# Performance work log

Measured on AMD Instinct MI355X. Metric: run time of the kernel, lower is better.

The kernel has to match this reference:

```python
import jax, jax.numpy as jnp
import numpy as np

N_NODES = 100000
N_EDGES = 1600000
N_IN = 64
N_OUT = 64


def setup_inputs() -> dict:
    key = jax.random.key(0)
    k_x, k_w, k_src, k_dst, k_val = jax.random.split(key, 5)
    X = jax.random.normal(k_x, (N_NODES, N_IN), dtype=jnp.float32)
    # Xavier-uniform init of the GCN weight matrix
    limit = float(np.sqrt(6.0 / (N_IN + N_OUT)))
    W = jax.random.uniform(k_w, (N_IN, N_OUT), dtype=jnp.float32,
                           minval=-limit, maxval=limit)
    # Sparse adjacency A in COO form: out[dst] += val * h[src]
    edge_src = jax.random.randint(k_src, (N_EDGES,), 0, N_NODES, dtype=jnp.int32)
    edge_dst = jax.random.randint(k_dst, (N_EDGES,), 0, N_NODES, dtype=jnp.int32)
    # normalized adjacency values (e.g., 1/sqrt(d_i d_j)); use uniform(0,1)
    edge_val = jax.random.uniform(k_val, (N_EDGES,), dtype=jnp.float32)
    return {"X": X, "W": W, "edge_val": edge_val,
            "edge_src": edge_src, "edge_dst": edge_dst}


def reference(X, W, edge_val, edge_src, edge_dst):
    # dropout p=0.0 -> identity (eval-mode math)
    h = X @ W                                   # [N, n_out] feature transform
    msgs = h[edge_src] * edge_val[:, None]      # [E, n_out] gather + scale
    agg = jax.ops.segment_sum(msgs, edge_dst, num_segments=N_NODES)  # A @ h
    return jax.nn.relu(agg)
```

## Files before the change

kernel.cpp:

```cpp
#include <hip/hip_runtime.h>
#include <hip/hip_bf16.h>

#define N_NODES 100000
#define N_IN    64
#define N_OUT   64
#define N_EDGES 1600000

#define BSHIFT  7
#define NPB     128
#define NB      782
#define CAP     2560
#define P1_EPT  16
#define P1_EPB  (256 * P1_EPT)
#define P1_BLOCKS ((N_EDGES + P1_EPB - 1) / P1_EPB)

__device__ inline unsigned short f2bf(float f) {
    __hip_bfloat16 b = __float2bfloat16(f);
    union { __hip_bfloat16 b; unsigned short u; } c; c.b = b; return c.u;
}

__global__ __launch_bounds__(256) void gemm_bf16_kernel(
        const float* __restrict__ X, const float* __restrict__ W,
        unsigned short* __restrict__ h) {
    __shared__ float Ws[N_IN * N_OUT];
    for (int i = threadIdx.x * 4; i < N_IN * N_OUT; i += 256 * 4)
        *(float4*)&Ws[i] = *(const float4*)&W[i];
    __syncthreads();

    const int r0 = blockIdx.x * 32 + (threadIdx.x >> 4) * 2;
    const int c0 = (threadIdx.x & 15) * 4;

    float acc0[4] = {0.f, 0.f, 0.f, 0.f};
    float acc1[4] = {0.f, 0.f, 0.f, 0.f};
    const float* x0p = X + (size_t)r0 * N_IN;
    const float* x1p = x0p + N_IN;

#pragma unroll 4
    for (int k4 = 0; k4 < 16; ++k4) {
        const float4 x0 = *(const float4*)(x0p + k4 * 4);
        const float4 x1 = *(const float4*)(x1p + k4 * 4);
        const float xa0[4] = {x0.x, x0.y, x0.z, x0.w};
        const float xa1[4] = {x1.x, x1.y, x1.z, x1.w};
#pragma unroll
        for (int kk = 0; kk < 4; ++kk) {
            const float4 w = *(const float4*)&Ws[(k4 * 4 + kk) * N_OUT + c0];
            acc0[0] = fmaf(xa0[kk], w.x, acc0[0]);
            acc0[1] = fmaf(xa0[kk], w.y, acc0[1]);
            acc0[2] = fmaf(xa0[kk], w.z, acc0[2]);
            acc0[3] = fmaf(xa0[kk], w.w, acc0[3]);
            acc1[0] = fmaf(xa1[kk], w.x, acc1[0]);
            acc1[1] = fmaf(xa1[kk], w.y, acc1[1]);
            acc1[2] = fmaf(xa1[kk], w.z, acc1[2]);
            acc1[3] = fmaf(xa1[kk], w.w, acc1[3]);
        }
    }
    ushort4 s0 = {f2bf(acc0[0]), f2bf(acc0[1]), f2bf(acc0[2]), f2bf(acc0[3])};
    ushort4 s1 = {f2bf(acc1[0]), f2bf(acc1[1]), f2bf(acc1[2]), f2bf(acc1[3])};
    *(ushort4*)&h[(size_t)r0 * N_OUT + c0] = s0;
    *(ushort4*)&h[(size_t)(r0 + 1) * N_OUT + c0] = s1;
}

__global__ __launch_bounds__(256) void bucket_kernel(
        const int* __restrict__ edge_src, const int* __restrict__ edge_dst,
        const float* __restrict__ edge_val,
        int* __restrict__ bucket_cursor, int2* __restrict__ staged) {
    __shared__ int cnt[NB];
    __shared__ int base[NB];
    const int t = threadIdx.x;
    for (int i = t; i < NB; i += 256) cnt[i] = 0;
    __syncthreads();

    const int e0 = blockIdx.x * P1_EPB + t * P1_EPT;
    const bool act = (e0 + P1_EPT) <= N_EDGES;
    int bk[P1_EPT], pk[P1_EPT], vv[P1_EPT];

    if (act) {
#pragma unroll
        for (int q = 0; q < P1_EPT / 4; ++q) {
            const int4 d4 = *(const int4*)(edge_dst + e0 + q * 4);
            const int4 s4 = *(const int4*)(edge_src + e0 + q * 4);
            const int4 v4 = *(const int4*)((const int*)edge_val + e0 + q * 4);
            const int da[4] = {d4.x, d4.y, d4.z, d4.w};
            const int sa[4] = {s4.x, s4.y, s4.z, s4.w};
            const int va[4] = {v4.x, v4.y, v4.z, v4.w};
#pragma unroll
            for (int j = 0; j < 4; ++j) {
                const int i = q * 4 + j;
                const int d = da[j];
                bk[i] = d >> BSHIFT;
                pk[i] = sa[j] | ((d & (NPB - 1)) << 17);
                vv[i] = va[j];
                atomicAdd(&cnt[bk[i]], 1);
            }
        }
    }
    __syncthreads();
    for (int i = t; i < NB; i += 256) {
        const int c = cnt[i];
        base[i] = c ? atomicAdd(&bucket_cursor[i], c) : 0;
        cnt[i] = 0;
    }
    __syncthreads();
    if (act) {
#pragma unroll
        for (int i = 0; i < P1_EPT; ++i) {
            const int b = bk[i];
            const int r = atomicAdd(&cnt[b], 1);
            const int pos = base[b] + r;
            if (pos < CAP) {
                int2 o; o.x = pk[i]; o.y = vv[i];
                staged[(size_t)b * CAP + pos] = o;
            }
        }
    }
}

__global__ __launch_bounds__(512) void sort_gather_kernel(
        const unsigned int* __restrict__ h32,
        const int2* __restrict__ staged,
        const int* __restrict__ bucket_cursor,
        float* __restrict__ out) {
    __shared__ int2 srt[CAP];
    __shared__ int  ncnt[NPB];
    __shared__ int  noff[NPB];
    const int t = threadIdx.x;
    const int b = blockIdx.x;
    const int cnt = min(bucket_cursor[b], CAP);
    const int2* bucket = staged + (size_t)b * CAP;

    if (t < NPB) ncnt[t] = 0;
    __syncthreads();
    for (int e = t; e < cnt; e += 512)
        atomicAdd(&ncnt[(unsigned)bucket[e].x >> 17], 1);
    __syncthreads();
    if (t < NPB) noff[t] = ncnt[t];
    __syncthreads();
    for (int d = 1; d < NPB; d <<= 1) {
        int x = 0;
        if (t < NPB && t >= d) x = noff[t - d];
        __syncthreads();
        if (t < NPB) noff[t] += x;
        __syncthreads();
    }
    if (t < NPB) {
        const int excl = noff[t] - ncnt[t];
        noff[t] = excl;
        ncnt[t] = excl;
    }
    __syncthreads();
    for (int e = t; e < cnt; e += 512) {
        const int2 p = bucket[e];
        const int node = (unsigned)p.x >> 17;
        const int pos = atomicAdd(&ncnt[node], 1);
        int2 o; o.x = p.x & 0x1FFFF; o.y = p.y;
        srt[pos] = o;
    }
    __syncthreads();

    const int w   = t >> 6;
    const int hf  = (t >> 5) & 1;
    const int i32 = t & 31;

    for (int nl = w * 16; nl < w * 16 + 16; ++nl) {
        const int node = b * NPB + nl;
        if (node >= N_NODES) break;
        const int s = noff[nl];
        const int e_end = ncnt[nl];

        float a0 = 0.f, a1 = 0.f;
        int e = s + hf;
        for (; e + 2 < e_end; e += 4) {
            const int2 p0 = srt[e];
            const int2 p1 = srt[e + 2];
            const unsigned int w0 = h32[(size_t)p0.x * 32 + i32];
            const unsigned int w1 = h32[(size_t)p1.x * 32 + i32];
            const float v0 = __int_as_float(p0.y);
            const float v1 = __int_as_float(p1.y);
            a0 = fmaf(__uint_as_float(w0 << 16), v0, a0);
            a1 = fmaf(__uint_as_float(w0 & 0xffff0000u), v0, a1);
            a0 = fmaf(__uint_as_float(w1 << 16), v1, a0);
            a1 = fmaf(__uint_as_float(w1 & 0xffff0000u), v1, a1);
        }
        for (; e < e_end; e += 2) {
            const int2 p = srt[e];
            const unsigned int w0 = h32[(size_t)p.x * 32 + i32];
            const float v = __int_as_float(p.y);
            a0 = fmaf(__uint_as_float(w0 << 16), v, a0);
            a1 = fmaf(__uint_as_float(w0 & 0xffff0000u), v, a1);
        }
        a0 += __shfl_xor(a0, 32, 64);
        a1 += __shfl_xor(a1, 32, 64);
        if (hf == 0) {
            float2 o;
            o.x = fmaxf(a0, 0.f);
            o.y = fmaxf(a1, 0.f);
            *(float2*)&out[(size_t)node * 64 + 2 * i32] = o;
        }
    }
}

__global__ __launch_bounds__(256) void gemm_f32_kernel(const float* __restrict__ X,
                                                       const float* __restrict__ W,
                                                       float* __restrict__ h) {
    __shared__ float Ws[N_IN * N_OUT];
    for (int i = threadIdx.x * 4; i < N_IN * N_OUT; i += 256 * 4)
        *(float4*)&Ws[i] = *(const float4*)&W[i];
    __syncthreads();
    const int lane = threadIdx.x & 63;
    const int wid = threadIdx.x >> 6;
    for (int row = blockIdx.x * 4 + wid; row < N_NODES; row += gridDim.x * 4) {
        const float x = X[row * N_IN + lane];
        float acc = 0.0f;
#pragma unroll
        for (int k = 0; k < N_IN; ++k)
            acc = fmaf(__shfl(x, k), Ws[k * N_OUT + lane], acc);
        h[row * N_OUT + lane] = acc;
    }
}

__global__ __launch_bounds__(256) void scatter_kernel(const float* __restrict__ h,
                                                      const float* __restrict__ edge_val,
                                                      const int* __restrict__ edge_src,
                                                      const int* __restrict__ edge_dst,
                                                      float* __restrict__ out) {
    const int lane = threadIdx.x & 63;
    const int e = (int)((blockIdx.x * 256u + threadIdx.x) >> 6);
    if (e >= N_EDGES) return;
    const float m = h[(size_t)edge_src[e] * N_OUT + lane] * edge_val[e];
    atomicAdd(&out[(size_t)edge_dst[e] * N_OUT + lane], m);
}

__global__ __launch_bounds__(256) void relu_kernel(float* __restrict__ out, int n) {
    const int i = (int)(blockIdx.x * 256u + threadIdx.x) * 4;
    if (i + 3 < n) {
        float4 v = *(float4*)&out[i];
        v.x = fmaxf(v.x, 0.f); v.y = fmaxf(v.y, 0.f);
        v.z = fmaxf(v.z, 0.f); v.w = fmaxf(v.w, 0.f);
        *(float4*)&out[i] = v;
    }
}

extern "C" void kernel_launch(void* const* d_in, const int* in_sizes, int n_in,
                              void* d_out, int out_size, void* d_ws, size_t ws_size,
                              hipStream_t stream) {
    const float* X        = (const float*)d_in[0];
    const float* W        = (const float*)d_in[1];
    const float* edge_val = (const float*)d_in[2];
    const int*   edge_src = (const int*)d_in[3];
    const int*   edge_dst = (const int*)d_in[4];
    float*       out      = (float*)d_out;

    unsigned short* h   = (unsigned short*)d_ws;
    int2* staged        = (int2*)((char*)d_ws + (size_t)N_NODES * N_OUT * 2);
    int*  bucket_cursor = (int*)(staged + (size_t)NB * CAP);
    const size_t need = (size_t)((char*)(bucket_cursor + NB) - (char*)d_ws);

    if (ws_size >= need) {
        hipMemsetAsync(bucket_cursor, 0, NB * sizeof(int), stream);
        gemm_bf16_kernel<<<N_NODES / 32, 256, 0, stream>>>(X, W, h);
        bucket_kernel<<<P1_BLOCKS, 256, 0, stream>>>(edge_src, edge_dst, edge_val,
                                                     bucket_cursor, staged);
        sort_gather_kernel<<<NB, 512, 0, stream>>>((const unsigned int*)h, staged,
                                                   bucket_cursor, out);
    } else {
        float* hf = (float*)d_ws;
        hipMemsetAsync(d_out, 0, (size_t)out_size * sizeof(float), stream);
        gemm_f32_kernel<<<25000, 256, 0, stream>>>(X, W, hf);
        const long long st = (long long)N_EDGES * 64;
        scatter_kernel<<<(int)((st + 255) / 256), 256, 0, stream>>>(
            hf, edge_val, edge_src, edge_dst, out);
        relu_kernel<<<(out_size / 4 + 255) / 256, 256, 0, stream>>>(out, out_size);
    }
}
```

Measured before the change: 173.4 us.

## Merge GEMM and bucketing into one launch; unroll gather loop deeper

The bf16 feature-transform GEMM and the edge bucketing pass are combined into a single prep kernel whose blocks branch on block index, with the bucketing blocks reusing the GEMM's shared weight buffer for their counters. This removes one kernel launch and lets the two independent phases run concurrently on the GPU instead of back to back. Separately, the gather loop in the sort/gather kernel is unrolled from two to four edges per iteration per half-wave, so more independent h loads are in flight. The wider unroll raises register pressure, and the mixed block types may balance unevenly across compute units.

```diff
diff --git a/kernel.cpp b/kernel.cpp
--- a/kernel.cpp
+++ b/kernel.cpp
@@ -13,103 +13,106 @@
 #define P1_EPT  16
 #define P1_EPB  (256 * P1_EPT)
 #define P1_BLOCKS ((N_EDGES + P1_EPB - 1) / P1_EPB)
+#define GEMM_BLOCKS (N_NODES / 32)
 
 __device__ inline unsigned short f2bf(float f) {
     __hip_bfloat16 b = __float2bfloat16(f);
     union { __hip_bfloat16 b; unsigned short u; } c; c.b = b; return c.u;
 }
 
-__global__ __launch_bounds__(256) void gemm_bf16_kernel(
+__global__ __launch_bounds__(256) void prep_kernel(
         const float* __restrict__ X, const float* __restrict__ W,
-        unsigned short* __restrict__ h) {
-    __shared__ float Ws[N_IN * N_OUT];
-    for (int i = threadIdx.x * 4; i < N_IN * N_OUT; i += 256 * 4)
-        *(float4*)&Ws[i] = *(const float4*)&W[i];
-    __syncthreads();
-
-    const int r0 = blockIdx.x * 32 + (threadIdx.x >> 4) * 2;
-    const int c0 = (threadIdx.x & 15) * 4;
-
-    float acc0[4] = {0.f, 0.f, 0.f, 0.f};
-    float acc1[4] = {0.f, 0.f, 0.f, 0.f};
-    const float* x0p = X + (size_t)r0 * N_IN;
-    const float* x1p = x0p + N_IN;
-
-#pragma unroll 4
-    for (int k4 = 0; k4 < 16; ++k4) {
-        const float4 x0 = *(const float4*)(x0p + k4 * 4);
-        const float4 x1 = *(const float4*)(x1p + k4 * 4);
-        const float xa0[4] = {x0.x, x0.y, x0.z, x0.w};
-        const float xa1[4] = {x1.x, x1.y, x1.z, x1.w};
-#pragma unroll
-        for (int kk = 0; kk < 4; ++kk) {
-            const float4 w = *(const float4*)&Ws[(k4 * 4 + kk) * N_OUT + c0];
-            acc0[0] = fmaf(xa0[kk], w.x, acc0[0]);
-            acc0[1] = fmaf(xa0[kk], w.y, acc0[1]);
-            acc0[2] = fmaf(xa0[kk], w.z, acc0[2]);
-            acc0[3] = fmaf(xa0[kk], w.w, acc0[3]);
-            acc1[0] = fmaf(xa1[kk], w.x, acc1[0]);
-            acc1[1] = fmaf(xa1[kk], w.y, acc1[1]);
-            acc1[2] = fmaf(xa1[kk], w.z, acc1[2]);
-            acc1[3] = fmaf(xa1[kk], w.w, acc1[3]);
-        }
-    }
-    ushort4 s0 = {f2bf(acc0[0]), f2bf(acc0[1]), f2bf(acc0[2]), f2bf(acc0[3])};
-    ushort4 s1 = {f2bf(acc1[0]), f2bf(acc1[1]), f2bf(acc1[2]), f2bf(acc1[3])};
-    *(ushort4*)&h[(size_t)r0 * N_OUT + c0] = s0;
-    *(ushort4*)&h[(size_t)(r0 + 1) * N_OUT + c0] = s1;
-}
-
-__global__ __launch_bounds__(256) void bucket_kernel(
+        unsigned short* __restrict__ h,
         const int* __restrict__ edge_src, const int* __restrict__ edge_dst,
         const float* __restrict__ edge_val,
         int* __restrict__ bucket_cursor, int2* __restrict__ staged) {
-    __shared__ int cnt[NB];
-    __shared__ int base[NB];
+    __shared__ float Ws[N_IN * N_OUT];
     const int t = threadIdx.x;
-    for (int i = t; i < NB; i += 256) cnt[i] = 0;
-    __syncthreads();
-
-    const int e0 = blockIdx.x * P1_EPB + t * P1_EPT;
-    const bool act = (e0 + P1_EPT) <= N_EDGES;
-    int bk[P1_EPT], pk[P1_EPT], vv[P1_EPT];
-
-    if (act) {
-#pragma unroll
-        for (int q = 0; q < P1_EPT / 4; ++q) {
-            const int4 d4 = *(const int4*)(edge_dst + e0 + q * 4);
-            const int4 s4 = *(const int4*)(edge_src + e0 + q * 4);
-            const int4 v4 = *(const int4*)((const int*)edge_val + e0 + q * 4);
-            const int da[4] = {d4.x, d4.y, d4.z, d4.w};
-            const int sa[4] = {s4.x, s4.y, s4.z, s4.w};
-            const int va[4] = {v4.x, v4.y, v4.z, v4.w};
-#pragma unroll
-            for (int j = 0; j < 4; ++j) {
-                const int i = q * 4 + j;
-                const int d = da[j];
-                bk[i] = d >> BSHIFT;
-                pk[i] = sa[j] | ((d & (NPB - 1)) << 17);
-                vv[i] = va[j];
-                atomicAdd(&cnt[bk[i]], 1);
+
+    if (blockIdx.x >= P1_BLOCKS) {
+        const int blk = blockIdx.x - P1_BLOCKS;
+        for (int i = t * 4; i < N_IN * N_OUT; i += 256 * 4)
+            *(float4*)&Ws[i] = *(const float4*)&W[i];
+        __syncthreads();
+
+        const int r0 = blk * 32 + (t >> 4) * 2;
+        const int c0 = (t & 15) * 4;
+
+        float acc0[4] = {0.f, 0.f, 0.f, 0.f};
+        float acc1[4] = {0.f, 0.f, 0.f, 0.f};
+        const float* x0p = X + (size_t)r0 * N_IN;
+        const float* x1p = x0p + N_IN;
+
+#pragma unroll 4
+        for (int k4 = 0; k4 < 16; ++k4) {
+            const float4 x0 = *(const float4*)(x0p + k4 * 4);
+            const float4 x1 = *(const float4*)(x1p + k4 * 4);
+            const float xa0[4] = {x0.x, x0.y, x0.z, x0.w};
+            const float xa1[4] = {x1.x, x1.y, x1.z, x1.w};
+#pragma unroll
+            for (int kk = 0; kk < 4; ++kk) {
+                const float4 w = *(const float4*)&Ws[(k4 * 4 + kk) * N_OUT + c0];
+                acc0[0] = fmaf(xa0[kk], w.x, acc0[0]);
+                acc0[1] = fmaf(xa0[kk], w.y, acc0[1]);
+                acc0[2] = fmaf(xa0[kk], w.z, acc0[2]);
+                acc0[3] = fmaf(xa0[kk], w.w, acc0[3]);
+                acc1[0] = fmaf(xa1[kk], w.x, acc1[0]);
+                acc1[1] = fmaf(xa1[kk], w.y, acc1[1]);
+                acc1[2] = fmaf(xa1[kk], w.z, acc1[2]);
+                acc1[3] = fmaf(xa1[kk], w.w, acc1[3]);
             }
         }
-    }
-    __syncthreads();
-    for (int i = t; i < NB; i += 256) {
-        const int c = cnt[i];
-        base[i] = c ? atomicAdd(&bucket_cursor[i], c) : 0;
-        cnt[i] = 0;
-    }
-    __syncthreads();
-    if (act) {
-#pragma unroll
-        for (int i = 0; i < P1_EPT; ++i) {
-            const int b = bk[i];
-            const int r = atomicAdd(&cnt[b], 1);
-            const int pos = base[b] + r;
-            if (pos < CAP) {
-                int2 o; o.x = pk[i]; o.y = vv[i];
-                staged[(size_t)b * CAP + pos] = o;
+        ushort4 s0 = {f2bf(acc0[0]), f2bf(acc0[1]), f2bf(acc0[2]), f2bf(acc0[3])};
+        ushort4 s1 = {f2bf(acc1[0]), f2bf(acc1[1]), f2bf(acc1[2]), f2bf(acc1[3])};
+        *(ushort4*)&h[(size_t)r0 * N_OUT + c0] = s0;
+        *(ushort4*)&h[(size_t)(r0 + 1) * N_OUT + c0] = s1;
+    } else {
+        int* cnt  = (int*)Ws;
+        int* base = cnt + NB;
+        for (int i = t; i < NB; i += 256) cnt[i] = 0;
+        __syncthreads();
+
+        const int e0 = blockIdx.x * P1_EPB + t * P1_EPT;
+        const bool act = (e0 + P1_EPT) <= N_EDGES;
+        int bk[P1_EPT], pk[P1_EPT], vv[P1_EPT];
+
+        if (act) {
+#pragma unroll
+            for (int q = 0; q < P1_EPT / 4; ++q) {
+                const int4 d4 = *(const int4*)(edge_dst + e0 + q * 4);
+                const int4 s4 = *(const int4*)(edge_src + e0 + q * 4);
+                const int4 v4 = *(const int4*)((const int*)edge_val + e0 + q * 4);
+                const int da[4] = {d4.x, d4.y, d4.z, d4.w};
+                const int sa[4] = {s4.x, s4.y, s4.z, s4.w};
+                const int va[4] = {v4.x, v4.y, v4.z, v4.w};
+#pragma unroll
+                for (int j = 0; j < 4; ++j) {
+                    const int i = q * 4 + j;
+                    const int d = da[j];
+                    bk[i] = d >> BSHIFT;
+                    pk[i] = sa[j] | ((d & (NPB - 1)) << 17);
+                    vv[i] = va[j];
+                    atomicAdd(&cnt[bk[i]], 1);
+                }
+            }
+        }
+        __syncthreads();
+        for (int i = t; i < NB; i += 256) {
+            const int c = cnt[i];
+            base[i] = c ? atomicAdd(&bucket_cursor[i], c) : 0;
+            cnt[i] = 0;
+        }
+        __syncthreads();
+        if (act) {
+#pragma unroll
+            for (int i = 0; i < P1_EPT; ++i) {
+                const int b = bk[i];
+                const int r = atomicAdd(&cnt[b], 1);
+                const int pos = base[b] + r;
+                if (pos < CAP) {
+                    int2 o; o.x = pk[i]; o.y = vv[i];
+                    staged[(size_t)b * CAP + pos] = o;
+                }
             }
         }
     }
@@ -169,17 +172,27 @@
 
         float a0 = 0.f, a1 = 0.f;
         int e = s + hf;
-        for (; e + 2 < e_end; e += 4) {
+        for (; e + 6 < e_end; e += 8) {
             const int2 p0 = srt[e];
             const int2 p1 = srt[e + 2];
+            const int2 p2 = srt[e + 4];
+            const int2 p3 = srt[e + 6];
             const unsigned int w0 = h32[(size_t)p0.x * 32 + i32];
             const unsigned int w1 = h32[(size_t)p1.x * 32 + i32];
+            const unsigned int w2 = h32[(size_t)p2.x * 32 + i32];
+            const unsigned int w3 = h32[(size_t)p3.x * 32 + i32];
             const float v0 = __int_as_float(p0.y);
             const float v1 = __int_as_float(p1.y);
+            const float v2 = __int_as_float(p2.y);
+            const float v3 = __int_as_float(p3.y);
             a0 = fmaf(__uint_as_float(w0 << 16), v0, a0);
             a1 = fmaf(__uint_as_float(w0 & 0xffff0000u), v0, a1);
             a0 = fmaf(__uint_as_float(w1 << 16), v1, a0);
             a1 = fmaf(__uint_as_float(w1 & 0xffff0000u), v1, a1);
+            a0 = fmaf(__uint_as_float(w2 << 16), v2, a0);
+            a1 = fmaf(__uint_as_float(w2 & 0xffff0000u), v2, a1);
+            a0 = fmaf(__uint_as_float(w3 << 16), v3, a0);
+            a1 = fmaf(__uint_as_float(w3 & 0xffff0000u), v3, a1);
         }
         for (; e < e_end; e += 2) {
             const int2 p = srt[e];
@@ -257,9 +270,8 @@
 
     if (ws_size >= need) {
         hipMemsetAsync(bucket_cursor, 0, NB * sizeof(int), stream);
-        gemm_bf16_kernel<<<N_NODES / 32, 256, 0, stream>>>(X, W, h);
-        bucket_kernel<<<P1_BLOCKS, 256, 0, stream>>>(edge_src, edge_dst, edge_val,
-                                                     bucket_cursor, staged);
+        prep_kernel<<<P1_BLOCKS + GEMM_BLOCKS, 256, 0, stream>>>(
+            X, W, h, edge_src, edge_dst, edge_val, bucket_cursor, staged);
         sort_gather_kernel<<<NB, 512, 0, stream>>>((const unsigned int*)h, staged,
                                                    bucket_cursor, out);
     } else {
```

Measured after the change: 168.6 us. -2.8%, faster.
